# Performance work log

Measured on AMD Instinct MI355X. Metric: run time of the kernel, lower is better.

The kernel has to match this reference:

```python
import jax, jax.numpy as jnp
import numpy as np

D = 1024
H = 16
HD = D // H
EPS = 1e-5
NEG = -1e20


def _layernorm(x, w, b):
    m = jnp.mean(x, axis=-1, keepdims=True)
    v = jnp.mean((x - m) ** 2, axis=-1, keepdims=True)
    return (x - m) * jax.lax.rsqrt(v + EPS) * w + b


def setup_inputs() -> dict:
    key = jax.random.key(0)
    ks = jax.random.split(key, 16)
    s = 0.02
    inp = {
        "X": jax.random.normal(ks[0], (2, 2048, D), jnp.float32),
        "Wq": jax.random.normal(ks[1], (D, D), jnp.float32) * s,
        "bq": jnp.zeros((D,), jnp.float32),
        "Wk": jax.random.normal(ks[2], (D, D), jnp.float32) * s,
        "bk": jnp.zeros((D,), jnp.float32),
        "Wv": jax.random.normal(ks[3], (D, D), jnp.float32) * s,
        "bv": jnp.zeros((D,), jnp.float32),
        "Wo": jax.random.normal(ks[4], (D, D), jnp.float32) * s,
        "bo": jnp.zeros((D,), jnp.float32),
        "ln1_w": jnp.ones((D,), jnp.float32),
        "ln1_b": jnp.zeros((D,), jnp.float32),
        "Wup": jax.random.normal(ks[5], (4 * D, D), jnp.float32) * s,
        "bup": jnp.zeros((4 * D,), jnp.float32),
        "Wdown": jax.random.normal(ks[6], (D, 4 * D), jnp.float32) * s,
        "bdown": jnp.zeros((D,), jnp.float32),
        "ln2_w": jnp.ones((D,), jnp.float32),
        "ln2_b": jnp.zeros((D,), jnp.float32),
    }
    return inp


def reference(X, Wq, bq, Wk, bk, Wv, bv, Wo, bo, ln1_w, ln1_b,
              Wup, bup, Wdown, bdown, ln2_w, ln2_b):
    B, S, _ = X.shape
    # QKV projections -> [B, H, S, HD]
    q = (X @ Wq.T + bq).reshape(B, S, H, HD).transpose(0, 2, 1, 3)
    k = (X @ Wk.T + bk).reshape(B, S, H, HD).transpose(0, 2, 1, 3)
    v = (X @ Wv.T + bv).reshape(B, S, H, HD).transpose(0, 2, 1, 3)
    scores = jnp.einsum("bhqd,bhkd->bhqk", q, k) / jnp.sqrt(jnp.float32(HD))
    causal = jnp.tril(jnp.ones((S, S), dtype=bool))  # mask==0 -> -1e20
    scores = jnp.where(causal, scores, jnp.float32(NEG))
    attn = jax.nn.softmax(scores, axis=-1)  # dropout is identity in eval
    out = jnp.einsum("bhqk,bhkd->bhqd", attn, v)
    out = out.transpose(0, 2, 1, 3).reshape(B, S, D)
    out = out @ Wo.T + bo
    x = _layernorm(X + out, ln1_w, ln1_b)  # post-LN attention block
    up = jax.nn.relu(x @ Wup.T + bup)
    down = up @ Wdown.T + bdown
    return _layernorm(x + down, ln2_w, ln2_b)
```

## Files before the change

kernel.cpp:

```cpp
#include <hip/hip_runtime.h>
#include <stdint.h>

#define DMODEL 1024
#define NHEAD 16
#define HDIM 64
#define SEQ 2048
#define NBATCH 2
#define MTOK 4096

typedef float f32x4 __attribute__((ext_vector_type(4)));
typedef short s16x8 __attribute__((ext_vector_type(8)));
typedef unsigned short u16;
typedef u16 u16x4 __attribute__((ext_vector_type(4)));

typedef __attribute__((address_space(1))) const void* as1_cvp;
typedef __attribute__((address_space(3))) void* as3_vp;

__device__ inline u16 f2bf(float f) {
  uint32_t u = __float_as_uint(f);
  u = u + 0x7FFFu + ((u >> 16) & 1u);
  return (u16)(u >> 16);
}

__device__ inline uint32_t pk_bf16(float lo, float hi) {
  uint32_t r;
  asm("v_cvt_pk_bf16_f32 %0, %1, %2" : "=v"(r) : "v"(lo), "v"(hi));
  return r;
}

__device__ inline void gload_lds16(const void* g, void* l) {
  __builtin_amdgcn_global_load_lds((as1_cvp)g, (as3_vp)l, 16, 0, 0);
}

__global__ __launch_bounds__(256) void k_f2bf(const float* __restrict__ src,
                                              u16* __restrict__ dst, int n4) {
  int i = blockIdx.x * 256 + threadIdx.x;
  int stride = gridDim.x * 256;
  for (; i < n4; i += stride) {
    f32x4 v = ((const f32x4*)src)[i];
    u16x4 o;
    o[0] = f2bf(v[0]); o[1] = f2bf(v[1]); o[2] = f2bf(v[2]); o[3] = f2bf(v[3]);
    ((u16x4*)dst)[i] = o;
  }
}

__global__ __launch_bounds__(256) void k_f2bf_w4(
    const float* __restrict__ s0, const float* __restrict__ s1,
    const float* __restrict__ s2, const float* __restrict__ s3,
    u16* __restrict__ d0, u16* __restrict__ d1, u16* __restrict__ d2,
    u16* __restrict__ d3, int n4) {
  const float* src = blockIdx.y == 0 ? s0 : blockIdx.y == 1 ? s1
                     : blockIdx.y == 2 ? s2 : s3;
  u16* dst = blockIdx.y == 0 ? d0 : blockIdx.y == 1 ? d1
             : blockIdx.y == 2 ? d2 : d3;
  int i = blockIdx.x * 256 + threadIdx.x;
  int stride = gridDim.x * 256;
  for (; i < n4; i += stride) {
    f32x4 v = ((const f32x4*)src)[i];
    u16x4 o;
    o[0] = f2bf(v[0]); o[1] = f2bf(v[1]); o[2] = f2bf(v[2]); o[3] = f2bf(v[3]);
    ((u16x4*)dst)[i] = o;
  }
}

template <int MODE, int KSPL, int MH>
__global__ __launch_bounds__(512, 2) void k_gemm256(
    const u16* __restrict__ A, const u16* __restrict__ B,
    const float* __restrict__ bias, void* __restrict__ Cv,
    void* __restrict__ Cv1, int M, int N, int K) {
  constexpr int HALVES = MH + 2;
  __shared__ alignas(16) u16 lds[2 * HALVES * 8192];
  const int t = threadIdx.x;
  const int w = t >> 6;
  const int l = t & 63;
  const int wr = w >> 2;
  const int wc = w & 3;
  const int lr = l & 15, lg = l >> 4;
  const int r7 = lr & 7;
  const int lrow8 = l >> 3;

  const int gx = gridDim.x;
  int lin = blockIdx.y * gx + blockIdx.x;
  const int nwg = gx * gridDim.y;
  lin = (lin & 7) * (nwg >> 3) + (lin >> 3);
  const int bx = lin % gx, by = lin / gx;
  const int kz = KSPL > 1 ? blockIdx.z : 0;
  const int Kc = K / KSPL, kbeg = kz * Kc;
  const int brow = by * (MH * 128), bcol = bx * 256;

  constexpr int MF = MH * 4;
  const f32x4 Z4 = {0.f, 0.f, 0.f, 0.f};
  f32x4 acc[MF][4];
#pragma unroll
  for (int m = 0; m < MF; m++)
#pragma unroll
    for (int n = 0; n < 4; n++) acc[m][n] = Z4;

  const u16* Ag = A + (size_t)brow * K + kbeg;
  const u16* Bg = B + (size_t)bcol * K + kbeg;
  const int swz_src = ((l & 7) ^ ((l >> 3) & 7)) << 3;

  auto ldsH = [&](int buf, int half) { return lds + (buf * HALVES + half) * 8192; };
  auto stageA = [&](int kt, int buf) {
#pragma unroll
    for (int h = 0; h < MH; h++) {
      u16* lb = ldsH(buf, h);
      const int rb = h * 128;
      gload_lds16(Ag + (size_t)(rb + w * 8 + lrow8) * K + kt * 64 + swz_src,
                  lb + w * 512);
      gload_lds16(Ag + (size_t)(rb + 64 + w * 8 + lrow8) * K + kt * 64 + swz_src,
                  lb + (8 + w) * 512);
    }
  };
  auto stageB = [&](int kt, int buf) {
#pragma unroll
    for (int h = 0; h < 2; h++) {
      u16* lb = ldsH(buf, MH + h);
      const int rb = h * 128;
      gload_lds16(Bg + (size_t)(rb + w * 8 + lrow8) * K + kt * 64 + swz_src,
                  lb + w * 512);
      gload_lds16(Bg + (size_t)(rb + 64 + w * 8 + lrow8) * K + kt * 64 + swz_src,
                  lb + (8 + w) * 512);
    }
  };

  stageA(0, 0);
  stageB(0, 0);

  const int nkt = Kc >> 6;
  const int arb = (MH == 2) ? 0 : wr * 64;
  const int brb = (wc & 1) * 64;
  for (int kt = 0; kt < nkt; ++kt) {
    const int cur = kt & 1, nx = cur ^ 1;
    if (kt + 1 < nkt) {
      stageA(kt + 1, nx);
      if (MH == 2)
        asm volatile("s_waitcnt vmcnt(4)" ::: "memory");
      else
        asm volatile("s_waitcnt vmcnt(2)" ::: "memory");
    } else {
      asm volatile("s_waitcnt vmcnt(0)" ::: "memory");
    }
    __builtin_amdgcn_s_barrier();
    __builtin_amdgcn_sched_barrier(0);
    const u16* Ah = ldsH(cur, (MH == 2) ? wr : 0);
    const u16* Bh = ldsH(cur, MH + (wc >> 1));
#pragma unroll
    for (int kk = 0; kk < 2; kk++) {
      s16x8 bfr[4];
#pragma unroll
      for (int nf = 0; nf < 4; nf++)
        bfr[nf] = *(const s16x8*)(Bh + (brb + nf * 16 + lr) * 64 +
                                  (((kk * 4 + lg) ^ r7) << 3));
#pragma unroll
      for (int mh = 0; mh < MH; mh++) {
        s16x8 afr[4];
#pragma unroll
        for (int i = 0; i < 4; i++)
          afr[i] = *(const s16x8*)(Ah + (arb + (mh * 4 + i) * 16 + lr) * 64 +
                                   (((kk * 4 + lg) ^ r7) << 3));
        __builtin_amdgcn_s_setprio(1);
#pragma unroll
        for (int i = 0; i < 4; i++)
#pragma unroll
          for (int nf = 0; nf < 4; nf++)
            acc[mh * 4 + i][nf] = __builtin_amdgcn_mfma_f32_16x16x32_bf16(
                afr[i], bfr[nf], acc[mh * 4 + i][nf], 0, 0, 0);
        __builtin_amdgcn_s_setprio(0);
      }
      if (kk == 0 && kt + 1 < nkt) stageB(kt + 1, nx);
    }
    __builtin_amdgcn_sched_barrier(0);
    __builtin_amdgcn_s_barrier();
  }

  const int lg4 = lg * 4;
  const int wrb = wr * (MH == 2 ? 128 : 64);
  if (MODE == 0) {
    float* Co = (kz == 0) ? (float*)Cv : (float*)Cv1;
#pragma unroll
    for (int nf = 0; nf < 4; nf++) {
      const int col = bcol + wc * 64 + nf * 16 + lr;
      const float bvv = (kz == 0) ? bias[col] : 0.0f;
#pragma unroll
      for (int mf = 0; mf < MF; mf++) {
        const int row0 = brow + wrb + mf * 16 + lg4;
#pragma unroll
        for (int r = 0; r < 4; r++)
          Co[(size_t)(row0 + r) * N + col] = acc[mf][nf][r] + bvv;
      }
    }
  } else {
    u16* Sgw = lds + w * 2176;
    float bn[4];
#pragma unroll
    for (int nf = 0; nf < 4; nf++) bn[nf] = bias[bcol + wc * 64 + nf * 16 + lr];
    const int ch = l & 7;
#pragma unroll
    for (int hh = 0; hh < MH * 2; hh++) {
#pragma unroll
      for (int mm = 0; mm < 2; mm++) {
        const int mf = hh * 2 + mm;
#pragma unroll
        for (int nf = 0; nf < 4; nf++)
#pragma unroll
          for (int r = 0; r < 4; r++) {
            float vv = acc[mf][nf][r] + bn[nf];
            if (MODE == 2) vv = vv > 0.f ? vv : 0.f;
            Sgw[(mm * 16 + lg4 + r) * 68 + nf * 16 + lr] = f2bf(vv);
          }
      }
#pragma unroll
      for (int i = 0; i < 4; i++) {
        const int rr = i * 8 + (l >> 3);
        u16x4 a0 = *(const u16x4*)(Sgw + rr * 68 + ch * 8);
        u16x4 a1 = *(const u16x4*)(Sgw + rr * 68 + ch * 8 + 4);
        s16x8 v8;
#pragma unroll
        for (int j = 0; j < 4; j++) { v8[j] = (short)a0[j]; v8[4 + j] = (short)a1[j]; }
        *(s16x8*)((u16*)Cv + (size_t)(brow + wrb + hh * 32 + rr) * N +
                  (bcol + wc * 64 + ch * 8)) = v8;
      }
    }
  }
}

__global__ __launch_bounds__(512, 2) void k_gemm256_qkv(
    const u16* __restrict__ A, const u16* __restrict__ B,
    const float* __restrict__ bq, const float* __restrict__ bk,
    const float* __restrict__ bv, u16* __restrict__ qbf, u16* __restrict__ kbf,
    u16* __restrict__ vtbf, int M, int N, int K) {
  __shared__ alignas(16) u16 lds[2 * 4 * 8192];
  const int t = threadIdx.x;
  const int w = t >> 6, l = t & 63;
  const int wr = w >> 2, wc = w & 3;
  const int lr = l & 15, lg = l >> 4;
  const int r7 = lr & 7;
  const int lrow8 = l >> 3;

  const int gx = gridDim.x;
  int lin = blockIdx.y * gx + blockIdx.x;
  const int nwg = gx * gridDim.y;
  lin = (lin & 7) * (nwg >> 3) + (lin >> 3);
  const int bx = lin % gx, by = lin / gx;
  const int brow = by * 256, bcol = bx * 256;

  const f32x4 Z4 = {0.f, 0.f, 0.f, 0.f};
  f32x4 acc[8][4];
#pragma unroll
  for (int m = 0; m < 8; m++)
#pragma unroll
    for (int n = 0; n < 4; n++) acc[m][n] = Z4;

  const u16* Ag = A + (size_t)brow * K;
  const u16* Bg = B + (size_t)bcol * K;
  const int swz_src = ((l & 7) ^ ((l >> 3) & 7)) << 3;

  auto ldsH = [&](int buf, int half) { return lds + (buf * 4 + half) * 8192; };
  auto stageA = [&](int kt, int buf) {
#pragma unroll
    for (int h = 0; h < 2; h++) {
      u16* lb = ldsH(buf, h);
      const int rb = h * 128;
      gload_lds16(Ag + (size_t)(rb + w * 8 + lrow8) * K + kt * 64 + swz_src,
                  lb + w * 512);
      gload_lds16(Ag + (size_t)(rb + 64 + w * 8 + lrow8) * K + kt * 64 + swz_src,
                  lb + (8 + w) * 512);
    }
  };
  auto stageB = [&](int kt, int buf) {
#pragma unroll
    for (int h = 0; h < 2; h++) {
      u16* lb = ldsH(buf, 2 + h);
      const int rb = h * 128;
      gload_lds16(Bg + (size_t)(rb + w * 8 + lrow8) * K + kt * 64 + swz_src,
                  lb + w * 512);
      gload_lds16(Bg + (size_t)(rb + 64 + w * 8 + lrow8) * K + kt * 64 + swz_src,
                  lb + (8 + w) * 512);
    }
  };

  stageA(0, 0);
  stageB(0, 0);

  const int nkt = K >> 6;
  const int brb = (wc & 1) * 64;
  for (int kt = 0; kt < nkt; ++kt) {
    const int cur = kt & 1, nx = cur ^ 1;
    if (kt + 1 < nkt) {
      stageA(kt + 1, nx);
      asm volatile("s_waitcnt vmcnt(4)" ::: "memory");
    } else {
      asm volatile("s_waitcnt vmcnt(0)" ::: "memory");
    }
    __builtin_amdgcn_s_barrier();
    __builtin_amdgcn_sched_barrier(0);
    const u16* Ah = ldsH(cur, wr);
    const u16* Bh = ldsH(cur, 2 + (wc >> 1));
#pragma unroll
    for (int kk = 0; kk < 2; kk++) {
      s16x8 bfr[4];
#pragma unroll
      for (int nf = 0; nf < 4; nf++)
        bfr[nf] = *(const s16x8*)(Bh + (brb + nf * 16 + lr) * 64 +
                                  (((kk * 4 + lg) ^ r7) << 3));
#pragma unroll
      for (int mh = 0; mh < 2; mh++) {
        s16x8 afr[4];
#pragma unroll
        for (int i = 0; i < 4; i++)
          afr[i] = *(const s16x8*)(Ah + ((mh * 4 + i) * 16 + lr) * 64 +
                                   (((kk * 4 + lg) ^ r7) << 3));
        __builtin_amdgcn_s_setprio(1);
#pragma unroll
        for (int i = 0; i < 4; i++)
#pragma unroll
          for (int nf = 0; nf < 4; nf++)
            acc[mh * 4 + i][nf] = __builtin_amdgcn_mfma_f32_16x16x32_bf16(
                afr[i], bfr[nf], acc[mh * 4 + i][nf], 0, 0, 0);
        __builtin_amdgcn_s_setprio(0);
      }
      if (kk == 0 && kt + 1 < nkt) stageB(kt + 1, nx);
    }
    __builtin_amdgcn_sched_barrier(0);
    __builtin_amdgcn_s_barrier();
  }

  const int lg4 = lg * 4;
  const int wrb = wr * 128;
  u16* Sgw = lds + w * 2176;
  const int colw = bcol + wc * 64;
  const int region = colw >> 10;
  const int ck0 = colw & 1023;
  float bn[4];
  {
    const float* bb = region == 0 ? bq : region == 1 ? bk : bv;
#pragma unroll
    for (int nf = 0; nf < 4; nf++) bn[nf] = bb[ck0 + nf * 16 + lr];
  }
  const int ch = l & 7;
  if (region <= 1) {
#pragma unroll
    for (int hh = 0; hh < 4; hh++) {
#pragma unroll
      for (int mm = 0; mm < 2; mm++) {
        const int mf = hh * 2 + mm;
#pragma unroll
        for (int nf = 0; nf < 4; nf++)
#pragma unroll
          for (int r = 0; r < 4; r++) {
            float vv = acc[mf][nf][r] + bn[nf];
            if (region == 0) vv *= 0.125f;
            Sgw[(mm * 16 + lg4 + r) * 68 + nf * 16 + lr] = f2bf(vv);
          }
      }
#pragma unroll
      for (int i = 0; i < 4; i++) {
        const int rr = i * 8 + (l >> 3);
        u16x4 a0 = *(const u16x4*)(Sgw + rr * 68 + ch * 8);
        u16x4 a1 = *(const u16x4*)(Sgw + rr * 68 + ch * 8 + 4);
        s16x8 v8;
#pragma unroll
        for (int j = 0; j < 4; j++) { v8[j] = (short)a0[j]; v8[4 + j] = (short)a1[j]; }
        const int tok = brow + wrb + hh * 32 + rr;
        if (region == 0)
          *(s16x8*)(qbf + (size_t)tok * 1024 + ck0 + ch * 8) = v8;
        else
          *(s16x8*)(kbf + (size_t)tok * 1024 + ck0 + (((ch ^ tok) & 7) << 3)) =
              v8;
      }
    }
  } else {
    const int hcol = ck0 >> 6;
#pragma unroll
    for (int dh = 0; dh < 2; dh++)
#pragma unroll
      for (int th = 0; th < 2; th++) {
#pragma unroll
        for (int nn = 0; nn < 2; nn++) {
          const int nf = dh * 2 + nn;
#pragma unroll
          for (int mi = 0; mi < 4; mi++) {
            const int mf = th * 4 + mi;
#pragma unroll
            for (int r = 0; r < 4; r++)
              Sgw[(nn * 16 + lr) * 68 + mi * 16 + lg4 + r] =
                  f2bf(acc[mf][nf][r] + bn[nf]);
          }
        }
#pragma unroll
        for (int i = 0; i < 4; i++) {
          const int rr = i * 8 + (l >> 3);
          u16x4 a0 = *(const u16x4*)(Sgw + rr * 68 + ch * 8);
          u16x4 a1 = *(const u16x4*)(Sgw + rr * 68 + ch * 8 + 4);
          s16x8 v8;
#pragma unroll
          for (int j = 0; j < 4; j++) { v8[j] = (short)a0[j]; v8[4 + j] = (short)a1[j]; }
          const int d = dh * 32 + rr;
          const int tokb = brow + wrb + th * 64 + ch * 8;
          const int b = tokb >> 11, s64b = tokb & 2047;
          const int ssb = (s64b & ~63) + ((((s64b >> 3) ^ d) & 7) << 3);
          *(s16x8*)(vtbf + ((size_t)((b << 4) + hcol) * 64 + d) * 2048 + ssb) =
              v8;
        }
      }
  }
}

__global__ __launch_bounds__(256, 2) void k_attn(const u16* __restrict__ q,
                                                 const u16* __restrict__ kk,
                                                 const u16* __restrict__ vt,
                                                 u16* __restrict__ o) {
  __shared__ alignas(16) u16 Ks[2][2][64 * 64];
  __shared__ alignas(16) u16 Vs[2][2][64 * 64];
  __shared__ alignas(16) u16 Ps[4][2][16 * 64];
  const int t = threadIdx.x;
  const int w = t >> 6;
  const int l = t & 63;
  const int idx = blockIdx.x;
  const int bh = idx & 31;
  const int p = idx >> 5;
  const int b = bh >> 4, h = bh & 15;
  const u16* qb = q + (size_t)b * SEQ * DMODEL + h * HDIM;
  const u16* kb = kk + (size_t)b * SEQ * DMODEL + h * HDIM;
  const u16* vb = vt + (size_t)((b * 16 + h) * 64) * SEQ;

  const int sr = t >> 3;
  const int sc = (t & 7) * 8;
  const int lr = l & 15, lg = l >> 4;
  const int key = lr & 7;
  const f32x4 Z4 = {0.f, 0.f, 0.f, 0.f};
  u16* PsBase = &Ps[0][0][0];
  u16* PsW = PsBase + w * 2048;

  for (int half = 0; half < 2; half++) {
    const int qt = half ? (31 - p) : p;
    const int nt = (qt >> 1) + 1;
    gload_lds16(qb + (size_t)(qt * 64 + w * 16 + (l >> 3)) * DMODEL + (l & 7) * 8,
                PsW);
    gload_lds16(
        qb + (size_t)(qt * 64 + w * 16 + 8 + (l >> 3)) * DMODEL + (l & 7) * 8,
        PsW + 512);
#pragma unroll
    for (int s = 0; s < 2; s++) {
      gload_lds16(kb + (size_t)(s * 64 + sr) * DMODEL + sc,
                  &Ks[0][s][0] + w * 512);
      gload_lds16(kb + (size_t)(s * 64 + sr + 32) * DMODEL + sc,
                  &Ks[0][s][0] + 2048 + w * 512);
      gload_lds16(vb + (size_t)sr * SEQ + s * 64 + sc, &Vs[0][s][0] + w * 512);
      gload_lds16(vb + (size_t)(sr + 32) * SEQ + s * 64 + sc,
                  &Vs[0][s][0] + 2048 + w * 512);
    }

    float m_l = -3.0e38f, l_l = 0.f;
    f32x4 oacc[4];
#pragma unroll
    for (int m = 0; m < 4; m++) oacc[m] = Z4;
    s16x8 bq0, bq1;

    for (int jt = 0; jt < nt; jt++) {
      const int cur = jt & 1;
      if (jt + 1 < nt) {
        const int nx = cur ^ 1;
        const int kvb = (jt + 1) * 128;
#pragma unroll
        for (int s = 0; s < 2; s++) {
          gload_lds16(kb + (size_t)(kvb + s * 64 + sr) * DMODEL + sc,
                      &Ks[nx][s][0] + w * 512);
          gload_lds16(kb + (size_t)(kvb + s * 64 + sr + 32) * DMODEL + sc,
                      &Ks[nx][s][0] + 2048 + w * 512);
          gload_lds16(vb + (size_t)sr * SEQ + kvb + s * 64 + sc,
                      &Vs[nx][s][0] + w * 512);
          gload_lds16(vb + (size_t)(sr + 32) * SEQ + kvb + s * 64 + sc,
                      &Vs[nx][s][0] + 2048 + w * 512);
        }
        asm volatile("s_waitcnt vmcnt(8)" ::: "memory");
      } else {
        asm volatile("s_waitcnt vmcnt(0)" ::: "memory");
      }
      __builtin_amdgcn_s_barrier();
      __builtin_amdgcn_sched_barrier(0);
      if (jt == 0) {
        bq0 = *(const s16x8*)(PsW + lr * 64 + lg * 8);
        bq1 = *(const s16x8*)(PsW + lr * 64 + 32 + lg * 8);
      }
      f32x4 sacc[8];
#pragma unroll
      for (int m = 0; m < 8; m++) sacc[m] = Z4;
#pragma unroll
      for (int m = 0; m < 8; m++) {
        const u16* Kc = &Ks[cur][m >> 2][0];
        const int rr = (m & 3) * 16 + lr;
        s16x8 ak0 = *(const s16x8*)(Kc + rr * 64 + ((lg ^ key) << 3));
        s16x8 ak1 = *(const s16x8*)(Kc + rr * 64 + (((4 | lg) ^ key) << 3));
        sacc[m] = __builtin_amdgcn_mfma_f32_16x16x32_bf16(ak0, bq0, sacc[m], 0, 0, 0);
        sacc[m] = __builtin_amdgcn_mfma_f32_16x16x32_bf16(ak1, bq1, sacc[m], 0, 0, 0);
      }
      if (jt == nt - 1) {
        const int qg = qt * 64 + w * 16 + lr - jt * 128;
#pragma unroll
        for (int m = 0; m < 8; m++)
#pragma unroll
          for (int r = 0; r < 4; r++)
            if (m * 16 + lg * 4 + r > qg) sacc[m][r] = -3.0e38f;
      }
      float mx[8];
#pragma unroll
      for (int m = 0; m < 8; m++)
        mx[m] = fmaxf(fmaxf(sacc[m][0], sacc[m][1]),
                      fmaxf(sacc[m][2], sacc[m][3]));
      float pmax = fmaxf(fmaxf(fmaxf(mx[0], mx[1]), fmaxf(mx[2], mx[3])),
                         fmaxf(fmaxf(mx[4], mx[5]), fmaxf(mx[6], mx[7])));
      pmax = fmaxf(pmax, __shfl_xor(pmax, 16, 64));
      pmax = fmaxf(pmax, __shfl_xor(pmax, 32, 64));
      if (!__all(pmax - m_l <= 8.0f)) {
        const float m_new = fmaxf(m_l, pmax);
        const float alpha = __expf(m_l - m_new);
        m_l = m_new;
        l_l *= alpha;
#pragma unroll
        for (int m = 0; m < 4; m++)
#pragma unroll
          for (int r = 0; r < 4; r++) oacc[m][r] *= alpha;
      }
      float p_[8][4], sm[8];
#pragma unroll
      for (int m = 0; m < 8; m++) {
#pragma unroll
        for (int r = 0; r < 4; r++) p_[m][r] = __expf(sacc[m][r] - m_l);
        sm[m] = (p_[m][0] + p_[m][1]) + (p_[m][2] + p_[m][3]);
      }
      float rs = ((sm[0] + sm[1]) + (sm[2] + sm[3])) +
                 ((sm[4] + sm[5]) + (sm[6] + sm[7]));
      rs += __shfl_xor(rs, 16, 64);
      rs += __shfl_xor(rs, 32, 64);
      l_l += rs;
#pragma unroll
      for (int m = 0; m < 8; m++)
#pragma unroll
        for (int pr = 0; pr < 2; pr++) {
          const uint32_t pk = pk_bf16(p_[m][2 * pr], p_[m][2 * pr + 1]);
          const int kv0 = m * 16 + lg * 4 + 2 * pr;
          const int sub = kv0 >> 6, kvp = kv0 & 63;
          ((uint32_t*)(PsW + sub * 1024))[lr * 32 + (((kvp >> 3) ^ key) << 2) +
                                          ((kvp >> 1) & 3)] = pk;
        }
      __builtin_amdgcn_sched_barrier(0);
#pragma unroll
      for (int ks = 0; ks < 4; ks++) {
        const int sub = ks >> 1;
        const int c = (ks & 1) * 4 + lg;
        s16x8 bp = *(const s16x8*)(PsW + sub * 1024 + lr * 64 + ((c ^ key) << 3));
        const u16* Vc = &Vs[cur][sub][0];
#pragma unroll
        for (int m = 0; m < 4; m++) {
          s16x8 av = *(const s16x8*)(Vc + (m * 16 + lr) * 64 + ((c ^ key) << 3));
          oacc[m] = __builtin_amdgcn_mfma_f32_16x16x32_bf16(av, bp, oacc[m], 0, 0, 0);
        }
      }
      __builtin_amdgcn_sched_barrier(0);
      __builtin_amdgcn_s_barrier();
    }
    const float rl = 1.0f / l_l;
    const int tok = qt * 64 + w * 16 + lr;
    u16* orow = o + (size_t)(b * SEQ + tok) * DMODEL + h * HDIM;
#pragma unroll
    for (int m = 0; m < 4; m++)
#pragma unroll
      for (int pr = 0; pr < 2; pr++) {
        const uint32_t pk =
            pk_bf16(oacc[m][2 * pr] * rl, oacc[m][2 * pr + 1] * rl);
        *(uint32_t*)(orow + m * 16 + lg * 4 + 2 * pr) = pk;
      }
  }
}

template <int XBF>
__global__ __launch_bounds__(256) void k_add_ln(const void* __restrict__ Xv,
                                                const float* __restrict__ Y,
                                                const float* __restrict__ Y1,
                                                const float* __restrict__ w,
                                                const float* __restrict__ bias,
                                                float* __restrict__ of32,
                                                u16* __restrict__ obf) {
  __shared__ float sred[4];
  const int t = threadIdx.x;
  const size_t row = blockIdx.x;
  f32x4 xv;
  if (XBF) {
    u16x4 xu = ((const u16x4*)((const u16*)Xv + row * DMODEL))[t];
    for (int i = 0; i < 4; i++)
      xv[i] = __uint_as_float((uint32_t)xu[i] << 16);
  } else {
    xv = ((const f32x4*)((const float*)Xv + row * DMODEL))[t];
  }
  f32x4 yv = ((const f32x4*)(Y + row * DMODEL))[t];
  f32x4 vv;
  for (int i = 0; i < 4; i++) vv[i] = xv[i] + yv[i];
  if (Y1) {
    f32x4 y1 = ((const f32x4*)(Y1 + row * DMODEL))[t];
    for (int i = 0; i < 4; i++) vv[i] += y1[i];
  }
  float s = vv[0] + vv[1] + vv[2] + vv[3];
  for (int off = 32; off >= 1; off >>= 1) s += __shfl_xor(s, off, 64);
  if ((t & 63) == 0) sred[t >> 6] = s;
  __syncthreads();
  s = sred[0] + sred[1] + sred[2] + sred[3];
  const float mean = s * (1.0f / DMODEL);
  f32x4 dv;
  for (int i = 0; i < 4; i++) dv[i] = vv[i] - mean;
  float ss = dv[0] * dv[0] + dv[1] * dv[1] + dv[2] * dv[2] + dv[3] * dv[3];
  __syncthreads();
  for (int off = 32; off >= 1; off >>= 1) ss += __shfl_xor(ss, off, 64);
  if ((t & 63) == 0) sred[t >> 6] = ss;
  __syncthreads();
  ss = sred[0] + sred[1] + sred[2] + sred[3];
  const float rs = rsqrtf(ss * (1.0f / DMODEL) + 1e-5f);
  f32x4 wv = ((const f32x4*)w)[t];
  f32x4 bv = ((const f32x4*)bias)[t];
  f32x4 ov;
  for (int i = 0; i < 4; i++) ov[i] = dv[i] * rs * wv[i] + bv[i];
  if (of32) ((f32x4*)(of32 + row * DMODEL))[t] = ov;
  if (obf) {
    u16x4 ob;
    for (int i = 0; i < 4; i++) ob[i] = f2bf(ov[i]);
    ((u16x4*)(obf + row * DMODEL))[t] = ob;
  }
}

extern "C" void kernel_launch(void* const* d_in, const int* in_sizes, int n_in,
                              void* d_out, int out_size, void* d_ws,
                              size_t ws_size, hipStream_t stream) {
  const float* X = (const float*)d_in[0];
  const float* Wq = (const float*)d_in[1];
  const float* bq = (const float*)d_in[2];
  const float* Wk = (const float*)d_in[3];
  const float* bk = (const float*)d_in[4];
  const float* Wv = (const float*)d_in[5];
  const float* bvp = (const float*)d_in[6];
  const float* Wo = (const float*)d_in[7];
  const float* bo = (const float*)d_in[8];
  const float* ln1w = (const float*)d_in[9];
  const float* ln1b = (const float*)d_in[10];
  const float* Wup = (const float*)d_in[11];
  const float* bup = (const float*)d_in[12];
  const float* Wdown = (const float*)d_in[13];
  const float* bdown = (const float*)d_in[14];
  const float* ln2w = (const float*)d_in[15];
  const float* ln2b = (const float*)d_in[16];

  char* ws = (char*)d_ws;
  const size_t MB = 1024 * 1024;
  u16* Xbf = (u16*)(ws + 0);
  u16* qbf = (u16*)(ws + 8 * MB);
  u16* kbf = (u16*)(ws + 16 * MB);
  u16* vtbf = (u16*)(ws + 24 * MB);
  u16* wqkv = (u16*)(ws + 32 * MB);
  u16* wo = (u16*)(ws + 38 * MB);
  u16* attnb = (u16*)(ws + 40 * MB);
  float* Ybuf = (float*)(ws + 48 * MB);
  u16* xbf = (u16*)(ws + 80 * MB);
  u16* upbf = (u16*)(ws + 0);
  u16* wbig = (u16*)(ws + 64 * MB);
  u16* wdownbf = attnb;
  float* Ypart = (float*)d_out;

  const dim3 blk(256);
  k_f2bf<<<2048, blk, 0, stream>>>(X, Xbf, (MTOK * DMODEL) / 4);
  k_f2bf_w4<<<dim3(512, 4), blk, 0, stream>>>(
      Wq, Wk, Wv, Wo, wqkv + 0 * 1024 * 1024, wqkv + 1 * 1024 * 1024,
      wqkv + 2 * 1024 * 1024, wo, (DMODEL * DMODEL) / 4);

  k_gemm256_qkv<<<dim3(12, 16), dim3(512), 0, stream>>>(
      Xbf, wqkv, bq, bk, bvp, qbf, kbf, vtbf, MTOK, 3 * DMODEL, DMODEL);
  k_attn<<<16 * NBATCH * NHEAD, blk, 0, stream>>>(qbf, kbf, vtbf, attnb);
  k_gemm256<0, 2, 1><<<dim3(4, 32, 2), dim3(512), 0, stream>>>(
      attnb, wo, bo, Ybuf, Ypart, MTOK, DMODEL, DMODEL);
  k_add_ln<0><<<MTOK, blk, 0, stream>>>(X, Ybuf, Ypart, ln1w, ln1b,
                                        (float*)nullptr, xbf);

  k_f2bf_w4<<<dim3(512, 4), blk, 0, stream>>>(
      Wup, Wup + 2 * 1024 * 1024, Wdown, Wdown + 2 * 1024 * 1024, wbig,
      wbig + 2 * 1024 * 1024, wdownbf, wdownbf + 2 * 1024 * 1024,
      (4 * DMODEL * DMODEL) / 8);
  k_gemm256<2, 1, 2><<<dim3(16, 16), dim3(512), 0, stream>>>(
      xbf, wbig, bup, upbf, nullptr, MTOK, 4 * DMODEL, DMODEL);
  k_gemm256<0, 2, 1><<<dim3(4, 32, 2), dim3(512), 0, stream>>>(
      upbf, wdownbf, bdown, Ybuf, Ypart, MTOK, DMODEL, 4 * DMODEL);
  k_add_ln<1><<<MTOK, blk, 0, stream>>>(xbf, Ybuf, Ypart, ln2w, ln2b,
                                        (float*)d_out, (u16*)nullptr);
}
```

Measured before the change: 200.4 us.

## Merge all fp32-to-bf16 conversions into one launch and widen attention blocks to 128 queries

All weight and input conversions now run in a single kernel with a 2D grid, replacing three separate launches. Wdown gets its own workspace region instead of aliasing the attention output buffer. The attention kernel moves to 512 threads with 8 waves covering a 128-query tile, halving the block count. Each K/V tile in shared memory is now shared by twice as many query rows, so each thread issues half as many loads. The trade-off is one block per CU, fewer blocks to balance the causal workload, and a coarser diagonal tile.

```diff
diff --git a/kernel.cpp b/kernel.cpp
--- a/kernel.cpp
+++ b/kernel.cpp
@@ -32,29 +32,31 @@
   __builtin_amdgcn_global_load_lds((as1_cvp)g, (as3_vp)l, 16, 0, 0);
 }
 
-__global__ __launch_bounds__(256) void k_f2bf(const float* __restrict__ src,
-                                              u16* __restrict__ dst, int n4) {
+__global__ __launch_bounds__(256) void k_f2bf_all(
+    const float* __restrict__ X, const float* __restrict__ Wq,
+    const float* __restrict__ Wk, const float* __restrict__ Wv,
+    const float* __restrict__ Wo, const float* __restrict__ Wup,
+    const float* __restrict__ Wdown, u16* __restrict__ dX,
+    u16* __restrict__ dqkv, u16* __restrict__ dwo, u16* __restrict__ dup,
+    u16* __restrict__ ddown) {
+  const int c = blockIdx.y;
+  const size_t CH = 1024 * 1024;
+  const float* src;
+  u16* dst;
+  if (c < 4) {
+    src = X + c * CH; dst = dX + c * CH;
+  } else if (c < 7) {
+    src = (c == 4 ? Wq : c == 5 ? Wk : Wv) ; dst = dqkv + (size_t)(c - 4) * CH;
+  } else if (c == 7) {
+    src = Wo; dst = dwo;
+  } else if (c < 12) {
+    src = Wup + (size_t)(c - 8) * CH; dst = dup + (size_t)(c - 8) * CH;
+  } else {
+    src = Wdown + (size_t)(c - 12) * CH; dst = ddown + (size_t)(c - 12) * CH;
+  }
+  const int n4 = (int)(CH / 4);
   int i = blockIdx.x * 256 + threadIdx.x;
-  int stride = gridDim.x * 256;
-  for (; i < n4; i += stride) {
-    f32x4 v = ((const f32x4*)src)[i];
-    u16x4 o;
-    o[0] = f2bf(v[0]); o[1] = f2bf(v[1]); o[2] = f2bf(v[2]); o[3] = f2bf(v[3]);
-    ((u16x4*)dst)[i] = o;
-  }
-}
-
-__global__ __launch_bounds__(256) void k_f2bf_w4(
-    const float* __restrict__ s0, const float* __restrict__ s1,
-    const float* __restrict__ s2, const float* __restrict__ s3,
-    u16* __restrict__ d0, u16* __restrict__ d1, u16* __restrict__ d2,
-    u16* __restrict__ d3, int n4) {
-  const float* src = blockIdx.y == 0 ? s0 : blockIdx.y == 1 ? s1
-                     : blockIdx.y == 2 ? s2 : s3;
-  u16* dst = blockIdx.y == 0 ? d0 : blockIdx.y == 1 ? d1
-             : blockIdx.y == 2 ? d2 : d3;
-  int i = blockIdx.x * 256 + threadIdx.x;
-  int stride = gridDim.x * 256;
+  const int stride = gridDim.x * 256;
   for (; i < n4; i += stride) {
     f32x4 v = ((const f32x4*)src)[i];
     u16x4 o;
@@ -407,13 +409,13 @@
   }
 }
 
-__global__ __launch_bounds__(256, 2) void k_attn(const u16* __restrict__ q,
+__global__ __launch_bounds__(512, 1) void k_attn(const u16* __restrict__ q,
                                                  const u16* __restrict__ kk,
                                                  const u16* __restrict__ vt,
                                                  u16* __restrict__ o) {
   __shared__ alignas(16) u16 Ks[2][2][64 * 64];
   __shared__ alignas(16) u16 Vs[2][2][64 * 64];
-  __shared__ alignas(16) u16 Ps[4][2][16 * 64];
+  __shared__ alignas(16) u16 Ps[8][2][16 * 64];
   const int t = threadIdx.x;
   const int w = t >> 6;
   const int l = t & 63;
@@ -430,26 +432,22 @@
   const int lr = l & 15, lg = l >> 4;
   const int key = lr & 7;
   const f32x4 Z4 = {0.f, 0.f, 0.f, 0.f};
-  u16* PsBase = &Ps[0][0][0];
-  u16* PsW = PsBase + w * 2048;
+  u16* PsW = &Ps[0][0][0] + w * 2048;
 
   for (int half = 0; half < 2; half++) {
-    const int qt = half ? (31 - p) : p;
-    const int nt = (qt >> 1) + 1;
-    gload_lds16(qb + (size_t)(qt * 64 + w * 16 + (l >> 3)) * DMODEL + (l & 7) * 8,
-                PsW);
+    const int qt = half ? (15 - p) : p;
+    const int nt = qt + 1;
     gload_lds16(
-        qb + (size_t)(qt * 64 + w * 16 + 8 + (l >> 3)) * DMODEL + (l & 7) * 8,
+        qb + (size_t)(qt * 128 + w * 16 + (l >> 3)) * DMODEL + (l & 7) * 8,
+        PsW);
+    gload_lds16(
+        qb + (size_t)(qt * 128 + w * 16 + 8 + (l >> 3)) * DMODEL + (l & 7) * 8,
         PsW + 512);
 #pragma unroll
     for (int s = 0; s < 2; s++) {
       gload_lds16(kb + (size_t)(s * 64 + sr) * DMODEL + sc,
                   &Ks[0][s][0] + w * 512);
-      gload_lds16(kb + (size_t)(s * 64 + sr + 32) * DMODEL + sc,
-                  &Ks[0][s][0] + 2048 + w * 512);
       gload_lds16(vb + (size_t)sr * SEQ + s * 64 + sc, &Vs[0][s][0] + w * 512);
-      gload_lds16(vb + (size_t)(sr + 32) * SEQ + s * 64 + sc,
-                  &Vs[0][s][0] + 2048 + w * 512);
     }
 
     float m_l = -3.0e38f, l_l = 0.f;
@@ -467,14 +465,10 @@
         for (int s = 0; s < 2; s++) {
           gload_lds16(kb + (size_t)(kvb + s * 64 + sr) * DMODEL + sc,
                       &Ks[nx][s][0] + w * 512);
-          gload_lds16(kb + (size_t)(kvb + s * 64 + sr + 32) * DMODEL + sc,
-                      &Ks[nx][s][0] + 2048 + w * 512);
           gload_lds16(vb + (size_t)sr * SEQ + kvb + s * 64 + sc,
                       &Vs[nx][s][0] + w * 512);
-          gload_lds16(vb + (size_t)(sr + 32) * SEQ + kvb + s * 64 + sc,
-                      &Vs[nx][s][0] + 2048 + w * 512);
         }
-        asm volatile("s_waitcnt vmcnt(8)" ::: "memory");
+        asm volatile("s_waitcnt vmcnt(4)" ::: "memory");
       } else {
         asm volatile("s_waitcnt vmcnt(0)" ::: "memory");
       }
@@ -497,7 +491,7 @@
         sacc[m] = __builtin_amdgcn_mfma_f32_16x16x32_bf16(ak1, bq1, sacc[m], 0, 0, 0);
       }
       if (jt == nt - 1) {
-        const int qg = qt * 64 + w * 16 + lr - jt * 128;
+        const int qg = qt * 128 + w * 16 + lr - jt * 128;
 #pragma unroll
         for (int m = 0; m < 8; m++)
 #pragma unroll
@@ -550,11 +544,13 @@
       for (int ks = 0; ks < 4; ks++) {
         const int sub = ks >> 1;
         const int c = (ks & 1) * 4 + lg;
-        s16x8 bp = *(const s16x8*)(PsW + sub * 1024 + lr * 64 + ((c ^ key) << 3));
+        s16x8 bp =
+            *(const s16x8*)(PsW + sub * 1024 + lr * 64 + ((c ^ key) << 3));
         const u16* Vc = &Vs[cur][sub][0];
 #pragma unroll
         for (int m = 0; m < 4; m++) {
-          s16x8 av = *(const s16x8*)(Vc + (m * 16 + lr) * 64 + ((c ^ key) << 3));
+          s16x8 av =
+              *(const s16x8*)(Vc + (m * 16 + lr) * 64 + ((c ^ key) << 3));
           oacc[m] = __builtin_amdgcn_mfma_f32_16x16x32_bf16(av, bp, oacc[m], 0, 0, 0);
         }
       }
@@ -562,7 +558,7 @@
       __builtin_amdgcn_s_barrier();
     }
     const float rl = 1.0f / l_l;
-    const int tok = qt * 64 + w * 16 + lr;
+    const int tok = qt * 128 + w * 16 + lr;
     u16* orow = o + (size_t)(b * SEQ + tok) * DMODEL + h * HDIM;
 #pragma unroll
     for (int m = 0; m < 4; m++)
@@ -659,30 +655,24 @@
   u16* wo = (u16*)(ws + 38 * MB);
   u16* attnb = (u16*)(ws + 40 * MB);
   float* Ybuf = (float*)(ws + 48 * MB);
+  u16* wbig = (u16*)(ws + 64 * MB);
+  u16* wdownbf = (u16*)(ws + 72 * MB);
   u16* xbf = (u16*)(ws + 80 * MB);
   u16* upbf = (u16*)(ws + 0);
-  u16* wbig = (u16*)(ws + 64 * MB);
-  u16* wdownbf = attnb;
   float* Ypart = (float*)d_out;
 
   const dim3 blk(256);
-  k_f2bf<<<2048, blk, 0, stream>>>(X, Xbf, (MTOK * DMODEL) / 4);
-  k_f2bf_w4<<<dim3(512, 4), blk, 0, stream>>>(
-      Wq, Wk, Wv, Wo, wqkv + 0 * 1024 * 1024, wqkv + 1 * 1024 * 1024,
-      wqkv + 2 * 1024 * 1024, wo, (DMODEL * DMODEL) / 4);
+  k_f2bf_all<<<dim3(128, 16), blk, 0, stream>>>(
+      X, Wq, Wk, Wv, Wo, Wup, Wdown, Xbf, wqkv, wo, wbig, wdownbf);
 
   k_gemm256_qkv<<<dim3(12, 16), dim3(512), 0, stream>>>(
       Xbf, wqkv, bq, bk, bvp, qbf, kbf, vtbf, MTOK, 3 * DMODEL, DMODEL);
-  k_attn<<<16 * NBATCH * NHEAD, blk, 0, stream>>>(qbf, kbf, vtbf, attnb);
+  k_attn<<<8 * NBATCH * NHEAD, dim3(512), 0, stream>>>(qbf, kbf, vtbf, attnb);
   k_gemm256<0, 2, 1><<<dim3(4, 32, 2), dim3(512), 0, stream>>>(
       attnb, wo, bo, Ybuf, Ypart, MTOK, DMODEL, DMODEL);
   k_add_ln<0><<<MTOK, blk, 0, stream>>>(X, Ybuf, Ypart, ln1w, ln1b,
                                         (float*)nullptr, xbf);
 
-  k_f2bf_w4<<<dim3(512, 4), blk, 0, stream>>>(
-      Wup, Wup + 2 * 1024 * 1024, Wdown, Wdown + 2 * 1024 * 1024, wbig,
-      wbig + 2 * 1024 * 1024, wdownbf, wdownbf + 2 * 1024 * 1024,
-      (4 * DMODEL * DMODEL) / 8);
   k_gemm256<2, 1, 2><<<dim3(16, 16), dim3(512), 0, stream>>>(
       xbf, wbig, bup, upbf, nullptr, MTOK, 4 * DMODEL, DMODEL);
   k_gemm256<0, 2, 1><<<dim3(4, 32, 2), dim3(512), 0, stream>>>(
```

Result: faster. 196.1 us (-2.1%).
